# Kernel optimization log

Hardware: AMD Instinct MI355X
Metric: run time of the kernel (lower is better)

The kernel has to match this reference:

```python
import jax, jax.numpy as jnp
import numpy as np

B, K, N, F, H = 20000, 10, 100000, 256, 128


def setup_inputs() -> dict:
    key = jax.random.key(0)
    ks = jax.random.split(key, 8)
    neighbors = jax.random.randint(ks[0], (B, K), 0, N)
    embed_table = jax.random.normal(ks[1], (N, F), dtype=jnp.float32)
    w = lambda k, shp: jax.random.normal(k, shp, dtype=jnp.float32) * 0.05
    return {
        "neighbors": neighbors,
        "embed_table": embed_table,
        "W1a": w(ks[2], (F, H)), "W1b": w(ks[3], (H, H)),
        "W2a": w(ks[4], (F, H)), "W2b": w(ks[5], (H, H)),
        "W3a": w(ks[6], (F, H)), "W3b": w(ks[7], (H, H)),
    }


def reference(neighbors, embed_table, W1a, W1b, W2a, W2b, W3a, W3b):
    # Gather each batch node's K sampled neighbor embeddings: [B, K, F]
    x = embed_table[neighbors]
    # Three MLP projections: Linear(F,H,no bias) -> tanh -> Linear(H,H,no bias)
    q = jnp.tanh(x @ W1a) @ W1b              # [B, K, H]  (att1)
    k = jnp.tanh(x @ W2a) @ W2b              # [B, K, H]  (att2)
    v = jnp.tanh(x @ W3a) @ W3b              # [B, K, H]  (att3)
    # Per-node attention over the K neighbors, softmax along last dim
    att = jax.nn.softmax(jnp.einsum('bid,bjd->bij', q, k), axis=-1)  # [B, K, K]
    # torch: sum over rows of (att @ v) -> contract both i and j
    out = jnp.einsum('bij,bjd->bd', att, v)  # [B, H]
    return out
```

## Files before the change

kernel.cpp:

```cpp
#include <hip/hip_runtime.h>
#include <hip/hip_bf16.h>

constexpr int B_ = 20000;
constexpr int K_ = 10;
constexpr int N_ = 100000;
constexpr int F_ = 256;
constexpr int H_ = 128;

typedef __attribute__((ext_vector_type(8))) short bf16x8;
typedef __attribute__((ext_vector_type(4))) float f32x4;
typedef __attribute__((ext_vector_type(4))) unsigned short ushort4v;

__device__ __forceinline__ unsigned short f2bf(float x) {
  unsigned int u = __builtin_bit_cast(unsigned int, x);
  unsigned int r = u + 0x7fffu + ((u >> 16) & 1u);
  return (unsigned short)(r >> 16);
}

__device__ __forceinline__ float fast_tanh(float x) {
  float e = __expf(2.0f * x);
  return 1.0f - 2.0f * __builtin_amdgcn_rcpf(e + 1.0f);
}

__global__ __launch_bounds__(256) void prep_kernel(
    const float* __restrict__ W1a, const float* __restrict__ W1b,
    const float* __restrict__ W2a, const float* __restrict__ W2b,
    const float* __restrict__ W3a, const float* __restrict__ W3b,
    unsigned short* __restrict__ wat, unsigned short* __restrict__ wbt) {
  const float* Wa[3] = {W1a, W2a, W3a};
  const float* Wb[3] = {W1b, W2b, W3b};
  int g = blockIdx.x * 256 + threadIdx.x;
  if (g < 3 * F_ * H_) {
    int p = g >> 15;
    int r = g & (F_ * H_ - 1);
    int h = r >> 8;
    int k = r & 255;
    wat[g] = f2bf(Wa[p][k * H_ + h]);
  } else {
    int g2 = g - 3 * F_ * H_;
    int p = g2 >> 14;
    int r = g2 & (H_ * H_ - 1);
    int h = r >> 7;
    int k = r & 127;
    wbt[g2] = f2bf(Wb[p][k * H_ + h]);
  }
}

constexpr int MT = 64;
constexpr int XS = F_ + 8;
constexpr int TS = H_ + 8;

__global__ __launch_bounds__(256, 3) void proj_kernel(
    const float* __restrict__ E,
    const unsigned short* __restrict__ wat,
    const unsigned short* __restrict__ wbt,
    unsigned short* __restrict__ qo, unsigned short* __restrict__ ko,
    unsigned short* __restrict__ vo) {
  __shared__ unsigned short xs[MT * XS];
  __shared__ unsigned short ts[MT * TS];

  const int tid = threadIdx.x;
  const int lane = tid & 63;
  const int w = tid >> 6;
  const int l15 = lane & 15;
  const int kg = lane >> 4;
  const int row0 = blockIdx.x * MT;

  {
    const float4* Eg = (const float4*)E;
#pragma unroll
    for (int it = 0; it < 16; ++it) {
      int i = tid + 256 * it;
      int r = i >> 6;
      int c4 = i & 63;
      float4 v = make_float4(0.f, 0.f, 0.f, 0.f);
      if (row0 + r < N_) v = Eg[(size_t)(row0 + r) * (F_ / 4) + c4];
      ushort4v o;
      o.x = f2bf(v.x); o.y = f2bf(v.y); o.z = f2bf(v.z); o.w = f2bf(v.w);
      *(ushort4v*)&xs[r * XS + c4 * 4] = o;
    }
  }
  __syncthreads();

  unsigned short* const outp[3] = {qo, ko, vo};

  for (int p = 0; p < 3; ++p) {
    const unsigned short* __restrict__ wap = wat + p * (F_ * H_);
    const unsigned short* __restrict__ wbp = wbt + p * (H_ * H_);

    f32x4 acc1[4][2];
#pragma unroll
    for (int rt = 0; rt < 4; ++rt)
#pragma unroll
      for (int c = 0; c < 2; ++c) acc1[rt][c] = (f32x4)0.0f;

#pragma unroll
    for (int k = 0; k < 8; ++k) {
      const int koff = k * 32 + kg * 8;
      bf16x8 b0 = *(const bf16x8*)&wap[(w * 32 + l15) * F_ + koff];
      bf16x8 b1 = *(const bf16x8*)&wap[(w * 32 + 16 + l15) * F_ + koff];
#pragma unroll
      for (int rt = 0; rt < 4; ++rt) {
        bf16x8 a = *(const bf16x8*)&xs[(rt * 16 + l15) * XS + koff];
        acc1[rt][0] = __builtin_amdgcn_mfma_f32_16x16x32_bf16(a, b0, acc1[rt][0], 0, 0, 0);
        acc1[rt][1] = __builtin_amdgcn_mfma_f32_16x16x32_bf16(a, b1, acc1[rt][1], 0, 0, 0);
      }
    }

    __syncthreads();
#pragma unroll
    for (int rt = 0; rt < 4; ++rt)
#pragma unroll
      for (int c = 0; c < 2; ++c)
#pragma unroll
        for (int r = 0; r < 4; ++r) {
          int m = rt * 16 + kg * 4 + r;
          int h = w * 32 + c * 16 + l15;
          ts[m * TS + h] = f2bf(fast_tanh(acc1[rt][c][r]));
        }
    __syncthreads();

    f32x4 acc2[4][2];
#pragma unroll
    for (int rt = 0; rt < 4; ++rt)
#pragma unroll
      for (int c = 0; c < 2; ++c) acc2[rt][c] = (f32x4)0.0f;

#pragma unroll
    for (int k = 0; k < 4; ++k) {
      const int koff = k * 32 + kg * 8;
      bf16x8 b0 = *(const bf16x8*)&wbp[(w * 32 + l15) * H_ + koff];
      bf16x8 b1 = *(const bf16x8*)&wbp[(w * 32 + 16 + l15) * H_ + koff];
#pragma unroll
      for (int rt = 0; rt < 4; ++rt) {
        bf16x8 a = *(const bf16x8*)&ts[(rt * 16 + l15) * TS + koff];
        acc2[rt][0] = __builtin_amdgcn_mfma_f32_16x16x32_bf16(a, b0, acc2[rt][0], 0, 0, 0);
        acc2[rt][1] = __builtin_amdgcn_mfma_f32_16x16x32_bf16(a, b1, acc2[rt][1], 0, 0, 0);
      }
    }

    unsigned short* __restrict__ o = outp[p];
#pragma unroll
    for (int rt = 0; rt < 4; ++rt)
#pragma unroll
      for (int c = 0; c < 2; ++c)
#pragma unroll
        for (int r = 0; r < 4; ++r) {
          int n = row0 + rt * 16 + kg * 4 + r;
          if (n < N_) o[(size_t)n * H_ + w * 32 + c * 16 + l15] = f2bf(acc2[rt][c][r]);
        }
  }
}

__global__ __launch_bounds__(128) void agg_kernel(
    const int* __restrict__ nbr,
    const __hip_bfloat16* __restrict__ qa,
    const __hip_bfloat16* __restrict__ ka,
    const __hip_bfloat16* __restrict__ va,
    float* __restrict__ out) {
  constexpr int RS = 132;
  __shared__ __align__(16) float qs[K_ * RS];
  __shared__ __align__(16) float ks[K_ * RS];
  __shared__ __align__(16) float vs[K_ * RS];
  __shared__ float sc[K_ * 12];
  __shared__ float colw[K_];
  const int b = blockIdx.x;
  const int tid = threadIdx.x;

  int nb[K_];
#pragma unroll
  for (int i = 0; i < K_; ++i) nb[i] = nbr[b * K_ + i];

#pragma unroll
  for (int i = 0; i < K_; ++i) {
    const int off = nb[i] * H_ + tid;
    qs[i * RS + tid] = __bfloat162float(qa[off]);
    ks[i * RS + tid] = __bfloat162float(ka[off]);
    vs[i * RS + tid] = __bfloat162float(va[off]);
  }
  __syncthreads();

  if (tid < K_ * K_) {
    const int i = tid / K_;
    const int j = tid - i * K_;
    const float4* q4 = (const float4*)&qs[i * RS];
    const float4* k4 = (const float4*)&ks[j * RS];
    float s = 0.0f;
#pragma unroll
    for (int d = 0; d < H_ / 4; ++d) {
      const float4 a = q4[d];
      const float4 c = k4[d];
      s = fmaf(a.x, c.x, s);
      s = fmaf(a.y, c.y, s);
      s = fmaf(a.z, c.z, s);
      s = fmaf(a.w, c.w, s);
    }
    sc[i * 12 + j] = s;
  }
  __syncthreads();

  if (tid < K_) {
    float m = sc[tid * 12 + 0];
#pragma unroll
    for (int j = 1; j < K_; ++j) m = fmaxf(m, sc[tid * 12 + j]);
    float e[K_];
    float sum = 0.0f;
#pragma unroll
    for (int j = 0; j < K_; ++j) {
      e[j] = __expf(sc[tid * 12 + j] - m);
      sum += e[j];
    }
    const float inv = __builtin_amdgcn_rcpf(sum);
#pragma unroll
    for (int j = 0; j < K_; ++j) sc[tid * 12 + j] = e[j] * inv;
  }
  __syncthreads();

  if (tid < K_) {
    float c = 0.0f;
#pragma unroll
    for (int i = 0; i < K_; ++i) c += sc[i * 12 + tid];
    colw[tid] = c;
  }
  __syncthreads();

  float o = 0.0f;
#pragma unroll
  for (int j = 0; j < K_; ++j) o = fmaf(colw[j], vs[j * RS + tid], o);
  out[(size_t)b * H_ + tid] = o;
}

extern "C" void kernel_launch(void* const* d_in, const int* in_sizes, int n_in,
                              void* d_out, int out_size, void* d_ws, size_t ws_size,
                              hipStream_t stream) {
  const int* nbr = (const int*)d_in[0];
  const float* E = (const float*)d_in[1];
  const float* W1a = (const float*)d_in[2];
  const float* W1b = (const float*)d_in[3];
  const float* W2a = (const float*)d_in[4];
  const float* W2b = (const float*)d_in[5];
  const float* W3a = (const float*)d_in[6];
  const float* W3b = (const float*)d_in[7];
  float* out = (float*)d_out;

  unsigned short* qa = (unsigned short*)d_ws;
  unsigned short* ka = qa + (size_t)N_ * H_;
  unsigned short* va = ka + (size_t)N_ * H_;
  unsigned short* wat = va + (size_t)N_ * H_;
  unsigned short* wbt = wat + (size_t)3 * F_ * H_;

  prep_kernel<<<(3 * F_ * H_ + 3 * H_ * H_) / 256, 256, 0, stream>>>(
      W1a, W1b, W2a, W2b, W3a, W3b, wat, wbt);
  proj_kernel<<<(N_ + MT - 1) / MT, 256, 0, stream>>>(E, wat, wbt, qa, ka, va);
  agg_kernel<<<B_, 128, 0, stream>>>(
      nbr, (const __hip_bfloat16*)qa, (const __hip_bfloat16*)ka,
      (const __hip_bfloat16*)va, out);
}
```

Baseline: 279.8 us.

## Shrink projection tile, preload weights to registers, rewrite aggregation with wave-level MFMA

The projection kernel now uses 32-row tiles and occupancy hint 4, preloads each projection's weight fragments into registers ahead of the MFMA loops, and drops bounds checks because N divides evenly. The aggregation kernel is rewritten so one wave handles one batch node. The 10x10 QK score matrix comes from MFMA on gathered bf16 rows, softmax and column sums use lane shuffles, and V is accumulated two elements per lane. This removes shared-memory staging and block barriers in aggregation and is meant to raise projection occupancy, at the cost of more weight-register pressure and padded-lane MFMA work.

New measurement: 285.1 us. Within noise of the previous version (+1.9%).

```diff
diff --git a/kernel.cpp b/kernel.cpp
--- a/kernel.cpp
+++ b/kernel.cpp
@@ -15,6 +15,10 @@
   unsigned int u = __builtin_bit_cast(unsigned int, x);
   unsigned int r = u + 0x7fffu + ((u >> 16) & 1u);
   return (unsigned short)(r >> 16);
+}
+
+__device__ __forceinline__ float bf2f(unsigned int u16) {
+  return __builtin_bit_cast(float, u16 << 16);
 }
 
 __device__ __forceinline__ float fast_tanh(float x) {
@@ -46,11 +50,11 @@
   }
 }
 
-constexpr int MT = 64;
+constexpr int MT = 32;
 constexpr int XS = F_ + 8;
 constexpr int TS = H_ + 8;
 
-__global__ __launch_bounds__(256, 3) void proj_kernel(
+__global__ __launch_bounds__(256, 4) void proj_kernel(
     const float* __restrict__ E,
     const unsigned short* __restrict__ wat,
     const unsigned short* __restrict__ wbt,
@@ -69,12 +73,11 @@
   {
     const float4* Eg = (const float4*)E;
 #pragma unroll
-    for (int it = 0; it < 16; ++it) {
+    for (int it = 0; it < 8; ++it) {
       int i = tid + 256 * it;
       int r = i >> 6;
       int c4 = i & 63;
-      float4 v = make_float4(0.f, 0.f, 0.f, 0.f);
-      if (row0 + r < N_) v = Eg[(size_t)(row0 + r) * (F_ / 4) + c4];
+      float4 v = Eg[(size_t)(row0 + r) * (F_ / 4) + c4];
       ushort4v o;
       o.x = f2bf(v.x); o.y = f2bf(v.y); o.z = f2bf(v.z); o.w = f2bf(v.w);
       *(ushort4v*)&xs[r * XS + c4 * 4] = o;
@@ -88,146 +91,150 @@
     const unsigned short* __restrict__ wap = wat + p * (F_ * H_);
     const unsigned short* __restrict__ wbp = wbt + p * (H_ * H_);
 
-    f32x4 acc1[4][2];
-#pragma unroll
-    for (int rt = 0; rt < 4; ++rt)
-#pragma unroll
-      for (int c = 0; c < 2; ++c) acc1[rt][c] = (f32x4)0.0f;
-
+    bf16x8 b1r[8][2];
 #pragma unroll
     for (int k = 0; k < 8; ++k) {
       const int koff = k * 32 + kg * 8;
-      bf16x8 b0 = *(const bf16x8*)&wap[(w * 32 + l15) * F_ + koff];
-      bf16x8 b1 = *(const bf16x8*)&wap[(w * 32 + 16 + l15) * F_ + koff];
-#pragma unroll
-      for (int rt = 0; rt < 4; ++rt) {
-        bf16x8 a = *(const bf16x8*)&xs[(rt * 16 + l15) * XS + koff];
-        acc1[rt][0] = __builtin_amdgcn_mfma_f32_16x16x32_bf16(a, b0, acc1[rt][0], 0, 0, 0);
-        acc1[rt][1] = __builtin_amdgcn_mfma_f32_16x16x32_bf16(a, b1, acc1[rt][1], 0, 0, 0);
-      }
-    }
+      b1r[k][0] = *(const bf16x8*)&wap[(w * 32 + l15) * F_ + koff];
+      b1r[k][1] = *(const bf16x8*)&wap[(w * 32 + 16 + l15) * F_ + koff];
+    }
+
+    f32x4 acc[2][2];
+#pragma unroll
+    for (int rt = 0; rt < 2; ++rt)
+#pragma unroll
+      for (int c = 0; c < 2; ++c) acc[rt][c] = (f32x4)0.0f;
+
+#pragma unroll
+    for (int k = 0; k < 8; ++k) {
+      const int koff = k * 32 + kg * 8;
+      bf16x8 a0 = *(const bf16x8*)&xs[l15 * XS + koff];
+      bf16x8 a1 = *(const bf16x8*)&xs[(16 + l15) * XS + koff];
+      acc[0][0] = __builtin_amdgcn_mfma_f32_16x16x32_bf16(a0, b1r[k][0], acc[0][0], 0, 0, 0);
+      acc[0][1] = __builtin_amdgcn_mfma_f32_16x16x32_bf16(a0, b1r[k][1], acc[0][1], 0, 0, 0);
+      acc[1][0] = __builtin_amdgcn_mfma_f32_16x16x32_bf16(a1, b1r[k][0], acc[1][0], 0, 0, 0);
+      acc[1][1] = __builtin_amdgcn_mfma_f32_16x16x32_bf16(a1, b1r[k][1], acc[1][1], 0, 0, 0);
+    }
+
+    bf16x8 b2r[4][2];
+#pragma unroll
+    for (int k = 0; k < 4; ++k) {
+      const int koff = k * 32 + kg * 8;
+      b2r[k][0] = *(const bf16x8*)&wbp[(w * 32 + l15) * H_ + koff];
+      b2r[k][1] = *(const bf16x8*)&wbp[(w * 32 + 16 + l15) * H_ + koff];
+    }
+
+    unsigned short tv[2][2][4];
+#pragma unroll
+    for (int rt = 0; rt < 2; ++rt)
+#pragma unroll
+      for (int c = 0; c < 2; ++c)
+#pragma unroll
+        for (int r = 0; r < 4; ++r)
+          tv[rt][c][r] = f2bf(fast_tanh(acc[rt][c][r]));
 
     __syncthreads();
 #pragma unroll
-    for (int rt = 0; rt < 4; ++rt)
+    for (int rt = 0; rt < 2; ++rt)
 #pragma unroll
       for (int c = 0; c < 2; ++c)
 #pragma unroll
-        for (int r = 0; r < 4; ++r) {
-          int m = rt * 16 + kg * 4 + r;
-          int h = w * 32 + c * 16 + l15;
-          ts[m * TS + h] = f2bf(fast_tanh(acc1[rt][c][r]));
-        }
+        for (int r = 0; r < 4; ++r)
+          ts[(rt * 16 + kg * 4 + r) * TS + w * 32 + c * 16 + l15] = tv[rt][c][r];
     __syncthreads();
 
-    f32x4 acc2[4][2];
-#pragma unroll
-    for (int rt = 0; rt < 4; ++rt)
-#pragma unroll
-      for (int c = 0; c < 2; ++c) acc2[rt][c] = (f32x4)0.0f;
+    f32x4 ac2[2][2];
+#pragma unroll
+    for (int rt = 0; rt < 2; ++rt)
+#pragma unroll
+      for (int c = 0; c < 2; ++c) ac2[rt][c] = (f32x4)0.0f;
 
 #pragma unroll
     for (int k = 0; k < 4; ++k) {
       const int koff = k * 32 + kg * 8;
-      bf16x8 b0 = *(const bf16x8*)&wbp[(w * 32 + l15) * H_ + koff];
-      bf16x8 b1 = *(const bf16x8*)&wbp[(w * 32 + 16 + l15) * H_ + koff];
-#pragma unroll
-      for (int rt = 0; rt < 4; ++rt) {
-        bf16x8 a = *(const bf16x8*)&ts[(rt * 16 + l15) * TS + koff];
-        acc2[rt][0] = __builtin_amdgcn_mfma_f32_16x16x32_bf16(a, b0, acc2[rt][0], 0, 0, 0);
-        acc2[rt][1] = __builtin_amdgcn_mfma_f32_16x16x32_bf16(a, b1, acc2[rt][1], 0, 0, 0);
-      }
+      bf16x8 a0 = *(const bf16x8*)&ts[l15 * TS + koff];
+      bf16x8 a1 = *(const bf16x8*)&ts[(16 + l15) * TS + koff];
+      ac2[0][0] = __builtin_amdgcn_mfma_f32_16x16x32_bf16(a0, b2r[k][0], ac2[0][0], 0, 0, 0);
+      ac2[0][1] = __builtin_amdgcn_mfma_f32_16x16x32_bf16(a0, b2r[k][1], ac2[0][1], 0, 0, 0);
+      ac2[1][0] = __builtin_amdgcn_mfma_f32_16x16x32_bf16(a1, b2r[k][0], ac2[1][0], 0, 0, 0);
+      ac2[1][1] = __builtin_amdgcn_mfma_f32_16x16x32_bf16(a1, b2r[k][1], ac2[1][1], 0, 0, 0);
     }
 
     unsigned short* __restrict__ o = outp[p];
 #pragma unroll
-    for (int rt = 0; rt < 4; ++rt)
+    for (int rt = 0; rt < 2; ++rt)
 #pragma unroll
       for (int c = 0; c < 2; ++c)
 #pragma unroll
         for (int r = 0; r < 4; ++r) {
           int n = row0 + rt * 16 + kg * 4 + r;
-          if (n < N_) o[(size_t)n * H_ + w * 32 + c * 16 + l15] = f2bf(acc2[rt][c][r]);
+          o[(size_t)n * H_ + w * 32 + c * 16 + l15] = f2bf(ac2[rt][c][r]);
         }
   }
 }
 
-__global__ __launch_bounds__(128) void agg_kernel(
+__global__ __launch_bounds__(256) void agg_kernel(
     const int* __restrict__ nbr,
-    const __hip_bfloat16* __restrict__ qa,
-    const __hip_bfloat16* __restrict__ ka,
-    const __hip_bfloat16* __restrict__ va,
+    const unsigned short* __restrict__ qa,
+    const unsigned short* __restrict__ ka,
+    const unsigned short* __restrict__ va,
     float* __restrict__ out) {
-  constexpr int RS = 132;
-  __shared__ __align__(16) float qs[K_ * RS];
-  __shared__ __align__(16) float ks[K_ * RS];
-  __shared__ __align__(16) float vs[K_ * RS];
-  __shared__ float sc[K_ * 12];
-  __shared__ float colw[K_];
-  const int b = blockIdx.x;
-  const int tid = threadIdx.x;
-
-  int nb[K_];
-#pragma unroll
-  for (int i = 0; i < K_; ++i) nb[i] = nbr[b * K_ + i];
-
-#pragma unroll
-  for (int i = 0; i < K_; ++i) {
-    const int off = nb[i] * H_ + tid;
-    qs[i * RS + tid] = __bfloat162float(qa[off]);
-    ks[i * RS + tid] = __bfloat162float(ka[off]);
-    vs[i * RS + tid] = __bfloat162float(va[off]);
-  }
-  __syncthreads();
-
-  if (tid < K_ * K_) {
-    const int i = tid / K_;
-    const int j = tid - i * K_;
-    const float4* q4 = (const float4*)&qs[i * RS];
-    const float4* k4 = (const float4*)&ks[j * RS];
-    float s = 0.0f;
-#pragma unroll
-    for (int d = 0; d < H_ / 4; ++d) {
-      const float4 a = q4[d];
-      const float4 c = k4[d];
-      s = fmaf(a.x, c.x, s);
-      s = fmaf(a.y, c.y, s);
-      s = fmaf(a.z, c.z, s);
-      s = fmaf(a.w, c.w, s);
-    }
-    sc[i * 12 + j] = s;
-  }
-  __syncthreads();
-
-  if (tid < K_) {
-    float m = sc[tid * 12 + 0];
-#pragma unroll
-    for (int j = 1; j < K_; ++j) m = fmaxf(m, sc[tid * 12 + j]);
-    float e[K_];
-    float sum = 0.0f;
-#pragma unroll
-    for (int j = 0; j < K_; ++j) {
-      e[j] = __expf(sc[tid * 12 + j] - m);
-      sum += e[j];
-    }
-    const float inv = __builtin_amdgcn_rcpf(sum);
-#pragma unroll
-    for (int j = 0; j < K_; ++j) sc[tid * 12 + j] = e[j] * inv;
-  }
-  __syncthreads();
-
-  if (tid < K_) {
-    float c = 0.0f;
-#pragma unroll
-    for (int i = 0; i < K_; ++i) c += sc[i * 12 + tid];
-    colw[tid] = c;
-  }
-  __syncthreads();
-
-  float o = 0.0f;
-#pragma unroll
-  for (int j = 0; j < K_; ++j) o = fmaf(colw[j], vs[j * RS + tid], o);
-  out[(size_t)b * H_ + tid] = o;
+  const int lane = threadIdx.x & 63;
+  const int wv = threadIdx.x >> 6;
+  const int b = blockIdx.x * 4 + wv;
+  const int l15 = lane & 15;
+  const int kg = lane >> 4;
+
+  const int ni = nbr[b * K_ + (l15 < K_ ? l15 : 0)];
+
+  f32x4 sc = (f32x4)0.0f;
+#pragma unroll
+  for (int k = 0; k < 4; ++k) {
+    const int off = k * 32 + kg * 8;
+    bf16x8 qf = *(const bf16x8*)&qa[(size_t)ni * H_ + off];
+    bf16x8 kf = *(const bf16x8*)&ka[(size_t)ni * H_ + off];
+    sc = __builtin_amdgcn_mfma_f32_16x16x32_bf16(qf, kf, sc, 0, 0, 0);
+  }
+
+  if (l15 >= K_) {
+#pragma unroll
+    for (int r = 0; r < 4; ++r) sc[r] = -3.0e38f;
+  }
+
+  float mx[4], e[4], sm[4];
+#pragma unroll
+  for (int r = 0; r < 4; ++r) mx[r] = sc[r];
+#pragma unroll
+  for (int st = 1; st < 16; st <<= 1)
+#pragma unroll
+    for (int r = 0; r < 4; ++r) mx[r] = fmaxf(mx[r], __shfl_xor(mx[r], st, 16));
+#pragma unroll
+  for (int r = 0; r < 4; ++r) { e[r] = __expf(sc[r] - mx[r]); sm[r] = e[r]; }
+#pragma unroll
+  for (int st = 1; st < 16; st <<= 1)
+#pragma unroll
+    for (int r = 0; r < 4; ++r) sm[r] += __shfl_xor(sm[r], st, 16);
+
+  float cs = 0.0f;
+#pragma unroll
+  for (int r = 0; r < 4; ++r) {
+    float a = e[r] * __builtin_amdgcn_rcpf(sm[r]);
+    if (kg * 4 + r >= K_) a = 0.0f;
+    cs += a;
+  }
+  cs += __shfl_xor(cs, 16, 64);
+  cs += __shfl_xor(cs, 32, 64);
+
+  float o0 = 0.0f, o1 = 0.0f;
+#pragma unroll
+  for (int j = 0; j < K_; ++j) {
+    const float cj = __shfl(cs, j, 64);
+    const int nj = __shfl(ni, j, 64);
+    const unsigned int v2 = *(const unsigned int*)&va[(size_t)nj * H_ + 2 * lane];
+    o0 = fmaf(cj, bf2f(v2 & 0xffffu), o0);
+    o1 = fmaf(cj, bf2f(v2 >> 16), o1);
+  }
+  *(float2*)&out[(size_t)b * H_ + 2 * lane] = make_float2(o0, o1);
 }
 
 extern "C" void kernel_launch(void* const* d_in, const int* in_sizes, int n_in,
@@ -251,8 +258,6 @@
 
   prep_kernel<<<(3 * F_ * H_ + 3 * H_ * H_) / 256, 256, 0, stream>>>(
       W1a, W1b, W2a, W2b, W3a, W3b, wat, wbt);
-  proj_kernel<<<(N_ + MT - 1) / MT, 256, 0, stream>>>(E, wat, wbt, qa, ka, va);
-  agg_kernel<<<B_, 128, 0, stream>>>(
-      nbr, (const __hip_bfloat16*)qa, (const __hip_bfloat16*)ka,
-      (const __hip_bfloat16*)va, out);
-}
+  proj_kernel<<<N_ / MT, 256, 0, stream>>>(E, wat, wbt, qa, ka, va);
+  agg_kernel<<<B_ / 4, 256, 0, stream>>>(nbr, qa, ka, va, out);
+}
```
